# Optimization experiments

Measured on AMD Instinct MI355X. Metric: run time of the kernel, lower is better.

## Reference

```python
import jax, jax.numpy as jnp
import numpy as np

DN = ('NCHW', 'OIHW', 'NCHW')

def conv2d(x, w, b):
    y = jax.lax.conv_general_dilated(x, w, (1, 1), 'SAME', dimension_numbers=DN)
    return y + b[None, :, None, None]

def deform_conv2d(x, offset, w, b):
    # torchvision DeformConv2d v1: kernel 3x3, stride 1, pad 1, dilation 1, no mask.
    # offset: [B, 18, H, W] ordered (dy0, dx0, dy1, dx1, ...) over row-major kernel taps.
    B, C, H, W = x.shape
    K2 = 9
    ki = (jnp.arange(K2) // 3).astype(x.dtype)  # kernel row index i
    kj = (jnp.arange(K2) % 3).astype(x.dtype)   # kernel col index j
    dy = offset[:, 0::2]  # [B, 9, H, W]
    dx = offset[:, 1::2]
    hh = jnp.arange(H, dtype=x.dtype)
    ww = jnp.arange(W, dtype=x.dtype)
    # sampling positions: p = out_pos - pad + k + offset
    py = hh[None, None, :, None] + ki[None, :, None, None] - 1.0 + dy  # [B,9,H,W]
    px = ww[None, None, None, :] + kj[None, :, None, None] - 1.0 + dx

    xf = x.reshape(B, C, H * W)
    y0 = jnp.floor(py); x0 = jnp.floor(px)
    y1 = y0 + 1.0;      x1 = x0 + 1.0
    wy1 = py - y0; wy0 = 1.0 - wy1
    wx1 = px - x0; wx0 = 1.0 - wx1

    def corner(yc, xc, cw):
        valid = (yc >= 0) & (yc <= H - 1) & (xc >= 0) & (xc <= W - 1)
        yi = jnp.clip(yc, 0, H - 1).astype(jnp.int32)
        xi = jnp.clip(xc, 0, W - 1).astype(jnp.int32)
        idx = yi * W + xi                       # [B,9,H,W]
        v = jax.vmap(lambda img, i: img[:, i])(xf, idx)  # [B,C,9,H,W]
        return v * (cw * valid.astype(x.dtype))[:, None]

    sampled = (corner(y0, x0, wy0 * wx0) + corner(y0, x1, wy0 * wx1)
               + corner(y1, x0, wy1 * wx0) + corner(y1, x1, wy1 * wx1))  # [B,C,9,H,W]
    out = jnp.einsum('bckhw,ock->bohw', sampled, w.reshape(w.shape[0], C, K2))
    return out + b[None, :, None, None]

def setup_inputs() -> dict:
    key = jax.random.key(0)
    ks = jax.random.split(key, 20)
    B, C, H, W = 8, 64, 128, 128
    O = 64
    s = 0.05
    inp = {
        'x': jax.random.normal(ks[0], (B, C, H, W), jnp.float32),
        'bsize': jax.random.uniform(ks[1], (B, 2), jnp.float32),
        # glob: Linear(2,64) -> ReLU -> Linear(64,32)
        'gw1': s * jax.random.normal(ks[2], (64, 2), jnp.float32),
        'gb1': jnp.zeros((64,), jnp.float32),
        'gw2': s * jax.random.normal(ks[3], (32, 64), jnp.float32),
        'gb2': jnp.zeros((32,), jnp.float32),
        # local: Conv2d(C,32,3) -> ReLU -> Conv2d(32,32,3)
        'lw1': s * jax.random.normal(ks[4], (32, C, 3, 3), jnp.float32),
        'lb1': jnp.zeros((32,), jnp.float32),
        'lw2': s * jax.random.normal(ks[5], (32, 32, 3, 3), jnp.float32),
        'lb2': jnp.zeros((32,), jnp.float32),
        # fuse: Conv2d(64,32,3) -> ReLU -> Conv2d(32,18,3)
        'fw1': s * jax.random.normal(ks[6], (32, 64, 3, 3), jnp.float32),
        'fb1': jnp.zeros((32,), jnp.float32),
        'fw2': s * jax.random.normal(ks[7], (18, 32, 3, 3), jnp.float32),
        'fb2': jnp.zeros((18,), jnp.float32),
        # deformable conv weight (copied from the source nn.Conv2d) + its own bias
        'dw': s * jax.random.normal(ks[8], (O, C, 3, 3), jnp.float32),
        'db': jnp.zeros((O,), jnp.float32),
    }
    return inp

def reference(x, bsize, gw1, gb1, gw2, gb2, lw1, lb1, lw2, lb2,
              fw1, fb1, fw2, fb2, dw, db):
    B, C, H, W = x.shape
    # global branch: MLP on box-size -> broadcast over spatial dims
    g = jax.nn.relu(bsize @ gw1.T + gb1) @ gw2.T + gb2          # [B,32]
    g_offset = jnp.broadcast_to(g[:, :, None, None], (B, 32, H, W))
    # local branch
    l_offset = conv2d(jax.nn.relu(conv2d(x, lw1, lb1)), lw2, lb2)  # [B,32,H,W]
    # fuse -> 18 offset channels
    fused = jnp.concatenate((g_offset, l_offset), axis=1)          # [B,64,H,W]
    offset = conv2d(jax.nn.relu(conv2d(fused, fw1, fb1)), fw2, fb2)  # [B,18,H,W]
    fea = deform_conv2d(x, offset, dw, db)
    return jax.nn.relu(fea)
```

## Files before the change

### kernel.cpp

```cpp
#include <hip/hip_runtime.h>

#define BB 8
#define CC 64
#define HH 128
#define WW 128
#define HWSZ (HH*WW)

typedef _Float16 h16;
typedef __attribute__((ext_vector_type(8))) _Float16 h16x8;
typedef __attribute__((ext_vector_type(4))) _Float16 h16x4;
typedef __attribute__((ext_vector_type(2))) _Float16 h16x2;
typedef __attribute__((ext_vector_type(4))) float f32x4;

typedef const __attribute__((address_space(1))) unsigned int* gptr_t;
typedef __attribute__((address_space(3))) unsigned int* lptr_t;

__device__ __forceinline__ void conv_pack(int j, int NCG, const float* w,
                                          int maxo, h16* dst) {
  int e = j & 7, l4 = (j >> 3) & 3, l15 = (j >> 5) & 15, f = (j >> 9) & 1;
  int cg = (j >> 10) & (NCG - 1), kt = (j >> 10) / NCG;
  int o = f * 16 + l15, c = cg * 32 + l4 * 8 + e;
  int CINw = NCG * 32;
  dst[j] = (o < maxo) ? (h16)w[(o * CINw + c) * 9 + kt] : (h16)0.f;
}

__global__ __launch_bounds__(256) void prep_kernel(
    const float* __restrict__ bsize, const float* __restrict__ gw1,
    const float* __restrict__ gb1, const float* __restrict__ gw2,
    const float* __restrict__ gb2, float* __restrict__ g,
    const float* __restrict__ lw1, const float* __restrict__ lw2,
    const float* __restrict__ fw1, const float* __restrict__ fw2,
    const float* __restrict__ dw, h16* __restrict__ cwq,
    h16* __restrict__ dwq, const float* __restrict__ x,
    h16* __restrict__ xt) {
  __shared__ float hbuf[BB][64];
  const int blk = blockIdx.x;
  const int tid = threadIdx.x;
  if (blk == 0) {
#pragma unroll
    for (int i2 = 0; i2 < 2; ++i2) {
      int idx = i2 * 256 + tid;
      int b = idx >> 6, i = idx & 63;
      float v = fmaf(bsize[b * 2 + 0], gw1[i * 2 + 0],
                     fmaf(bsize[b * 2 + 1], gw1[i * 2 + 1], gb1[i]));
      hbuf[b][i] = fmaxf(v, 0.f);
    }
    __syncthreads();
    int b = tid >> 5, j = tid & 31;
    float acc = gb2[j];
#pragma unroll
    for (int i = 0; i < 64; ++i) acc = fmaf(hbuf[b][i], gw2[j * 64 + i], acc);
    g[b * 32 + j] = acc;
  } else if (blk <= 360) {
    int i = (blk - 1) * 256 + tid;
    if (i < 18432) {
      conv_pack(i, 2, lw1, 32, cwq);
    } else if (i < 27648) {
      conv_pack(i - 18432, 1, lw2, 32, cwq + 18432);
    } else if (i < 46080) {
      conv_pack(i - 27648, 2, fw1, 32, cwq + 27648);
    } else if (i < 55296) {
      conv_pack(i - 46080, 1, fw2, 18, cwq + 46080);
    } else if (i < 55296 + 36864) {
      int j = i - 55296;
      int e = j & 7, l4 = (j >> 3) & 3, l15 = (j >> 5) & 15;
      int og = (j >> 9) & 3, cg = (j >> 11) & 1, kt = j >> 12;
      int o = og * 16 + l15, c = cg * 32 + l4 * 8 + e;
      dwq[j] = (h16)dw[(o * 64 + c) * 9 + kt];
    }
  } else {
    int j = blk - 361;
    int b = (1 + j) & 7;
    int slot = j >> 3;
    int t = b * 16384 + slot * 256 + tid;
    int p = t & 16383;
    const float* xb = x + (size_t)b * 64 * HWSZ + p;
    h16* ob = xt + (size_t)t * 64;
#pragma unroll
    for (int c0 = 0; c0 < 64; c0 += 8) {
      h16x8 v;
#pragma unroll
      for (int i = 0; i < 8; ++i) v[i] = (h16)xb[(size_t)(c0 + i) * HWSZ];
      *(h16x8*)(ob + c0) = v;
    }
  }
}

template <int NCG, bool GFUSE, bool RELU, int OMODE>
__global__ __launch_bounds__(512) void conv_mfma_kernel(
    const h16* __restrict__ in, const h16* __restrict__ cwq,
    const float* __restrict__ bias, const float* __restrict__ g,
    h16* __restrict__ outv) {
  constexpr int CINS = GFUSE ? 32 : NCG * 32;
  constexpr int NS = CINS / 8;
  constexpr int LOG2NS = (NS == 8) ? 3 : 2;
  constexpr int NCHUNK = 4 * 128 * NS;
  __shared__ __align__(16) h16 sh[4 * 128 * CINS];
  const int wgid = (blockIdx.x & 7) * 64 + (blockIdx.x >> 3);
  const int b = wgid >> 6;
  const int h0 = (wgid & 63) * 2;
  const int lane = threadIdx.x & 63, wave = threadIdx.x >> 6;
  const int wr = wave >> 2, wv = wave & 3;
  const int h = h0 + wr;
  const int l15 = lane & 15, l4 = lane >> 4;
  const h16* inb = in + (size_t)b * HWSZ * CINS;

#pragma unroll
  for (int it = 0; it < NCHUNK / 512; ++it) {
    int q = it * 512 + threadIdx.x;
    int sp = q & (NS - 1), pr = q >> LOG2NS;
    int r = pr >> 7, px = pr & 127;
    int gy = min(max(h0 - 1 + r, 0), HH - 1);
    int s = sp ^ (px & (NS - 1));
    const h16* src = inb + ((size_t)gy * WW + px) * CINS + s * 8;
    __builtin_amdgcn_global_load_lds(
        (gptr_t)src, (lptr_t)(sh + (size_t)(it * 512 + wave * 64) * 8), 16, 0, 0);
  }

  const h16x8 zfr = {0, 0, 0, 0, 0, 0, 0, 0};
  h16x8 gfr = zfr;
  if (GFUSE) {
#pragma unroll
    for (int i = 0; i < 8; ++i) gfr[i] = (h16)g[b * 32 + l4 * 8 + i];
  }
  __syncthreads();

  f32x4 acc[2][2];
#pragma unroll
  for (int f = 0; f < 2; ++f)
#pragma unroll
    for (int j = 0; j < 2; ++j) acc[f][j] = (f32x4){0.f, 0.f, 0.f, 0.f};

#pragma unroll
  for (int kt = 0; kt < 9; ++kt) {
    const int ki = kt / 3 - 1, kj = kt % 3 - 1;
    const int y = h + ki;
    const bool yok = (unsigned)y < HH;
    const int r = ki + 1 + wr;
    int xs[2];
    bool ok[2];
#pragma unroll
    for (int j = 0; j < 2; ++j) {
      int xx = wv * 32 + j * 16 + l15 + kj;
      ok[j] = yok && ((unsigned)xx < WW);
      xs[j] = min(max(xx, 0), WW - 1);
    }
#pragma unroll
    for (int cg = 0; cg < NCG; ++cg) {
      const h16* aq = cwq + (size_t)((kt * NCG + cg) * 2) * 512 + l15 * 32 + l4 * 8;
      h16x8 afr0 = *(const h16x8*)(aq);
      h16x8 afr1 = *(const h16x8*)(aq + 512);
#pragma unroll
      for (int j = 0; j < 2; ++j) {
        h16x8 bv;
        if (GFUSE && cg == 0) {
          bv = ok[j] ? gfr : zfr;
        } else {
          const int s = (!GFUSE && NCG == 2) ? cg * 4 + l4 : l4;
          h16x8 ld = *(const h16x8*)(sh + (r * 128 + xs[j]) * CINS +
                                     ((s ^ (xs[j] & (NS - 1))) * 8));
          bv = ok[j] ? ld : zfr;
        }
        acc[0][j] = __builtin_amdgcn_mfma_f32_16x16x32_f16(afr0, bv, acc[0][j], 0, 0, 0);
        acc[1][j] = __builtin_amdgcn_mfma_f32_16x16x32_f16(afr1, bv, acc[1][j], 0, 0, 0);
      }
    }
  }
  if (OMODE == 0) {
    h16* ob = outv + (size_t)b * HWSZ * 32;
#pragma unroll
    for (int f = 0; f < 2; ++f)
#pragma unroll
      for (int j = 0; j < 2; ++j) {
        int p = h * WW + wv * 32 + j * 16 + l15;
        int o0 = f * 16 + l4 * 4;
        h16x4 st;
#pragma unroll
        for (int r2 = 0; r2 < 4; ++r2) {
          float v = acc[f][j][r2] + bias[o0 + r2];
          if (RELU) v = fmaxf(v, 0.f);
          st[r2] = (h16)v;
        }
        *(h16x4*)(ob + (size_t)p * 32 + o0) = st;
      }
  } else {
    h16* ob = outv + (size_t)b * HWSZ * 24;
#pragma unroll
    for (int j = 0; j < 2; ++j) {
      int p = h * WW + wv * 32 + j * 16 + l15;
      {
        int o0 = l4 * 4;
        h16x4 st;
#pragma unroll
        for (int r2 = 0; r2 < 4; ++r2) st[r2] = (h16)(acc[0][j][r2] + bias[o0 + r2]);
        *(h16x4*)(ob + (size_t)p * 24 + o0) = st;
      }
      if (l4 == 0) {
        h16x2 st2;
        st2[0] = (h16)(acc[1][j][0] + bias[16]);
        st2[1] = (h16)(acc[1][j][1] + bias[17]);
        *(h16x2*)(ob + (size_t)p * 24 + 16) = st2;
      }
    }
  }
}

__global__ __launch_bounds__(256) void deform_mfma_kernel(
    const h16* __restrict__ xt, const h16* __restrict__ offc,
    const h16* __restrict__ dwq, const float* __restrict__ db,
    float* __restrict__ out) {
  __shared__ __align__(16) h16 sh[5 * 72 * 64];
  const int wgid = (blockIdx.x & 7) * 256 + (blockIdx.x >> 3);
  const int b = wgid >> 8;
  const int rh = wgid & 255;
  const int h = rh >> 1;
  const int halfx = (rh & 1) * 64;
  const int x_lo = halfx - 4;
  const int lane = threadIdx.x & 63, wave = threadIdx.x >> 6;
  const int l15 = lane & 15, l4 = lane >> 4;
  const int wx = halfx + wave * 16;
  const int p0 = h * WW + wx;
  const int myw = wx + l15;
  const int mypix = p0 + l15;
  const h16* xb = xt + (size_t)b * HWSZ * 64;

#pragma unroll
  for (int it = 0; it < 12; ++it) {
    int q = it * 256 + threadIdx.x;
    if (q < 2880) {
      int sp = q & 7, pr = q >> 3;
      int r = pr / 72, i = pr - r * 72;
      int gy = min(max(h - 2 + r, 0), HH - 1);
      int gx = min(max(x_lo + i, 0), WW - 1);
      int s = sp ^ (i & 7);
      const h16* src = xb + ((size_t)gy * WW + gx) * 64 + s * 8;
      __builtin_amdgcn_global_load_lds(
          (gptr_t)src, (lptr_t)(sh + (size_t)(it * 256 + wave * 64) * 8), 16, 0, 0);
    }
  }

  const h16* offp = offc + ((size_t)b * HWSZ + mypix) * 24;
  h16x8 offv0 = *(const h16x8*)(offp);
  h16x8 offv1 = *(const h16x8*)(offp + 8);
  h16x8 offv2 = *(const h16x8*)(offp + 16);
  __syncthreads();

#define OFFE(e) ((e) < 8 ? (float)offv0[(e) & 7] : (e) < 16 ? (float)offv1[(e) & 7] : (float)offv2[(e) & 7])

  f32x4 acc[4];
#pragma unroll
  for (int og = 0; og < 4; ++og) acc[og] = (f32x4){0.f, 0.f, 0.f, 0.f};

  h16x8 pc[2][2][4];
  h16x8 pw[2][8];
  h16   pg[2][4];

#define PREF(kt, par) do {                                                  \
    float py = (float)(h + (kt) / 3 - 1) + OFFE(2 * (kt));                  \
    float px = (float)(myw + (kt) % 3 - 1) + OFFE(2 * (kt) + 1);            \
    float y0f = floorf(py), x0f = floorf(px);                               \
    float wy1 = py - y0f, wy0 = 1.f - wy1;                                  \
    float wx1 = px - x0f, wx0 = 1.f - wx1;                                  \
    int y0 = (int)y0f, x0i = (int)x0f;                                      \
    int y1 = y0 + 1, x1i = x0i + 1;                                         \
    bool y0ok = (unsigned)y0 < HH, y1ok = (unsigned)y1 < HH;                \
    bool x0ok = (unsigned)x0i < WW, x1ok = (unsigned)x1i < WW;              \
    pg[par][0] = (h16)((y0ok && x0ok) ? wy0 * wx0 : 0.f);                   \
    pg[par][1] = (h16)((y0ok && x1ok) ? wy0 * wx1 : 0.f);                   \
    pg[par][2] = (h16)((y1ok && x0ok) ? wy1 * wx0 : 0.f);                   \
    pg[par][3] = (h16)((y1ok && x1ok) ? wy1 * wx1 : 0.f);                   \
    int y0c = min(max(y0, 0), HH - 1), y1c = min(max(y1, 0), HH - 1);       \
    int x0c = min(max(x0i, 0), WW - 1), x1c = min(max(x1i, 0), WW - 1);     \
    int ty0u = y0c - (h - 2), ty1u = y1c - (h - 2);                         \
    int tx0u = x0c - x_lo, tx1u = x1c - x_lo;                               \
    bool fast = ((unsigned)ty0u <= 4u) & ((unsigned)ty1u <= 4u) &           \
                ((unsigned)tx0u <= 71u) & ((unsigned)tx1u <= 71u);          \
    int ty0 = min(max(ty0u, 0), 4), ty1 = min(max(ty1u, 0), 4);             \
    int tx0 = min(max(tx0u, 0), 71), tx1 = min(max(tx1u, 0), 71);           \
    int pr00 = (ty0 * 72 + tx0) * 64, pr01 = (ty0 * 72 + tx1) * 64;         \
    int pr10 = (ty1 * 72 + tx0) * 64, pr11 = (ty1 * 72 + tx1) * 64;         \
    int sx0 = (tx0 & 7) * 8, sx1 = (tx1 & 7) * 8;                           \
    _Pragma("unroll")                                                       \
    for (int cg = 0; cg < 2; ++cg) {                                        \
      int sb = (cg * 4 + l4) * 8;                                           \
      pc[par][cg][0] = *(const h16x8*)(sh + pr00 + (sb ^ sx0));             \
      pc[par][cg][1] = *(const h16x8*)(sh + pr01 + (sb ^ sx1));             \
      pc[par][cg][2] = *(const h16x8*)(sh + pr10 + (sb ^ sx0));             \
      pc[par][cg][3] = *(const h16x8*)(sh + pr11 + (sb ^ sx1));             \
    }                                                                       \
    if (!fast) {                                                            \
      int i00 = y0c * WW + x0c, i01 = y0c * WW + x1c;                       \
      int i10 = y1c * WW + x0c, i11 = y1c * WW + x1c;                       \
      _Pragma("unroll")                                                     \
      for (int cg = 0; cg < 2; ++cg) {                                      \
        const h16* cb = xb + cg * 32 + l4 * 8;                              \
        pc[par][cg][0] = *(const h16x8*)(cb + (size_t)i00 * 64);            \
        pc[par][cg][1] = *(const h16x8*)(cb + (size_t)i01 * 64);            \
        pc[par][cg][2] = *(const h16x8*)(cb + (size_t)i10 * 64);            \
        pc[par][cg][3] = *(const h16x8*)(cb + (size_t)i11 * 64);            \
      }                                                                     \
    }                                                                       \
    const h16* wq0 = dwq + ((size_t)((kt) * 2 + 0) * 64 + l15) * 32 + l4 * 8; \
    const h16* wq1 = dwq + ((size_t)((kt) * 2 + 1) * 64 + l15) * 32 + l4 * 8; \
    pw[par][0] = *(const h16x8*)(wq0 + 0 * 512);                            \
    pw[par][1] = *(const h16x8*)(wq0 + 1 * 512);                            \
    pw[par][2] = *(const h16x8*)(wq0 + 2 * 512);                            \
    pw[par][3] = *(const h16x8*)(wq0 + 3 * 512);                            \
    pw[par][4] = *(const h16x8*)(wq1 + 0 * 512);                            \
    pw[par][5] = *(const h16x8*)(wq1 + 1 * 512);                            \
    pw[par][6] = *(const h16x8*)(wq1 + 2 * 512);                            \
    pw[par][7] = *(const h16x8*)(wq1 + 3 * 512);                            \
  } while (0)

#define CONS(par) do {                                                      \
    h16 w00 = pg[par][0], w01 = pg[par][1], w10 = pg[par][2], w11 = pg[par][3]; \
    h16x8 s0 = pc[par][0][0] * w00 + pc[par][0][1] * w01                    \
             + pc[par][0][2] * w10 + pc[par][0][3] * w11;                   \
    h16x8 s1 = pc[par][1][0] * w00 + pc[par][1][1] * w01                    \
             + pc[par][1][2] * w10 + pc[par][1][3] * w11;                   \
    acc[0] = __builtin_amdgcn_mfma_f32_16x16x32_f16(s0, pw[par][0], acc[0], 0, 0, 0); \
    acc[1] = __builtin_amdgcn_mfma_f32_16x16x32_f16(s0, pw[par][1], acc[1], 0, 0, 0); \
    acc[2] = __builtin_amdgcn_mfma_f32_16x16x32_f16(s0, pw[par][2], acc[2], 0, 0, 0); \
    acc[3] = __builtin_amdgcn_mfma_f32_16x16x32_f16(s0, pw[par][3], acc[3], 0, 0, 0); \
    acc[0] = __builtin_amdgcn_mfma_f32_16x16x32_f16(s1, pw[par][4], acc[0], 0, 0, 0); \
    acc[1] = __builtin_amdgcn_mfma_f32_16x16x32_f16(s1, pw[par][5], acc[1], 0, 0, 0); \
    acc[2] = __builtin_amdgcn_mfma_f32_16x16x32_f16(s1, pw[par][6], acc[2], 0, 0, 0); \
    acc[3] = __builtin_amdgcn_mfma_f32_16x16x32_f16(s1, pw[par][7], acc[3], 0, 0, 0); \
  } while (0)

  PREF(0, 0);
  PREF(1, 1);
  CONS(0);
  PREF(2, 0);
  CONS(1);
  PREF(3, 1);
  CONS(0);
  PREF(4, 0);
  CONS(1);
  PREF(5, 1);
  CONS(0);
  PREF(6, 0);
  CONS(1);
  PREF(7, 1);
  CONS(0);
  PREF(8, 0);
  CONS(1);
  CONS(0);
#undef PREF
#undef CONS
#undef OFFE

  float* outb = out + (size_t)b * CC * HWSZ;
#pragma unroll
  for (int og = 0; og < 4; ++og) {
    int o = og * 16 + l15;
    float bv = db[o];
    f32x4 st;
#pragma unroll
    for (int r = 0; r < 4; ++r) st[r] = fmaxf(acc[og][r] + bv, 0.f);
    *(f32x4*)(outb + (size_t)o * HWSZ + p0 + l4 * 4) = st;
  }
}

extern "C" void kernel_launch(void* const* d_in, const int* in_sizes, int n_in,
                              void* d_out, int out_size, void* d_ws, size_t ws_size,
                              hipStream_t stream) {
  const float* x     = (const float*)d_in[0];
  const float* bsize = (const float*)d_in[1];
  const float* gw1   = (const float*)d_in[2];
  const float* gb1   = (const float*)d_in[3];
  const float* gw2   = (const float*)d_in[4];
  const float* gb2   = (const float*)d_in[5];
  const float* lw1   = (const float*)d_in[6];
  const float* lb1   = (const float*)d_in[7];
  const float* lw2   = (const float*)d_in[8];
  const float* lb2   = (const float*)d_in[9];
  const float* fw1   = (const float*)d_in[10];
  const float* fb1   = (const float*)d_in[11];
  const float* fw2   = (const float*)d_in[12];
  const float* fb2   = (const float*)d_in[13];
  const float* dw    = (const float*)d_in[14];
  const float* db    = (const float*)d_in[15];
  float* out = (float*)d_out;

  float* gbuf = (float*)d_ws;
  h16* xt   = (h16*)((char*)d_ws + 2048);
  h16* offc = (h16*)((char*)d_ws + 2048 + (size_t)BB * HWSZ * 64 * 2);
  h16* dwq  = (h16*)((char*)offc + (size_t)BB * HWSZ * 24 * 2);

  h16* loff = (h16*)d_out;
  h16* cwq  = (h16*)d_out + 4194304;
  h16* t12  = (h16*)d_out + 8388608;
  const h16* lw1q = cwq;
  const h16* lw2q = cwq + 18432;
  const h16* fw1q = cwq + 27648;
  const h16* fw2q = cwq + 46080;

  prep_kernel<<<873, 256, 0, stream>>>(bsize, gw1, gb1, gw2, gb2, gbuf,
                                       lw1, lw2, fw1, fw2, dw, cwq, dwq, x, xt);
  conv_mfma_kernel<2, false, true, 0><<<512, 512, 0, stream>>>(
      xt, lw1q, lb1, nullptr, t12);
  conv_mfma_kernel<1, false, false, 0><<<512, 512, 0, stream>>>(
      t12, lw2q, lb2, nullptr, loff);
  conv_mfma_kernel<2, true, true, 0><<<512, 512, 0, stream>>>(
      loff, fw1q, fb1, gbuf, t12);
  conv_mfma_kernel<1, false, false, 1><<<512, 512, 0, stream>>>(
      t12, fw2q, fb2, nullptr, offc);
  deform_mfma_kernel<<<2048, 256, 0, stream>>>(xt, offc, dwq, db, out);
}
```

Baseline: 102.1 us.

## Fuse final offset conv into deformable conv kernel when workspace allows

The last 3x3 conv producing the 18 offset channels is computed inside the deformable conv kernel. Each block stages a 3-row halo of the 32-channel intermediate into LDS, runs MFMAs against packed fw2 weights, and passes the offsets through shared memory. This removes one kernel launch and the write and re-read of the offset tensor. In exchange it adds extra LDS, barriers and some halo recompute to the deform kernel, and it only takes effect if the workspace is large enough.

```diff
diff --git a/kernel.cpp b/kernel.cpp
--- a/kernel.cpp
+++ b/kernel.cpp
@@ -31,8 +31,8 @@
     const float* __restrict__ lw1, const float* __restrict__ lw2,
     const float* __restrict__ fw1, const float* __restrict__ fw2,
     const float* __restrict__ dw, h16* __restrict__ cwq,
-    h16* __restrict__ dwq, const float* __restrict__ x,
-    h16* __restrict__ xt) {
+    h16* __restrict__ dwq, h16* __restrict__ fw2w,
+    const float* __restrict__ x, h16* __restrict__ xt) {
   __shared__ float hbuf[BB][64];
   const int blk = blockIdx.x;
   const int tid = threadIdx.x;
@@ -61,6 +61,7 @@
       conv_pack(i - 27648, 2, fw1, 32, cwq + 27648);
     } else if (i < 55296) {
       conv_pack(i - 46080, 1, fw2, 18, cwq + 46080);
+      conv_pack(i - 46080, 1, fw2, 18, fw2w);
     } else if (i < 55296 + 36864) {
       int j = i - 55296;
       int e = j & 7, l4 = (j >> 3) & 3, l15 = (j >> 5) & 15;
@@ -205,11 +206,14 @@
   }
 }
 
+template <bool FUSED>
 __global__ __launch_bounds__(256) void deform_mfma_kernel(
-    const h16* __restrict__ xt, const h16* __restrict__ offc,
+    const h16* __restrict__ xt, const h16* __restrict__ aux,
     const h16* __restrict__ dwq, const float* __restrict__ db,
+    const h16* __restrict__ fw2q, const float* __restrict__ fb2,
     float* __restrict__ out) {
   __shared__ __align__(16) h16 sh[5 * 72 * 64];
+  __shared__ __align__(16) h16 sh2[FUSED ? 3 * 72 * 32 : 8];
   const int wgid = (blockIdx.x & 7) * 256 + (blockIdx.x >> 3);
   const int b = wgid >> 8;
   const int rh = wgid & 255;
@@ -223,6 +227,7 @@
   const int myw = wx + l15;
   const int mypix = p0 + l15;
   const h16* xb = xt + (size_t)b * HWSZ * 64;
+  const h16x8 zfr8 = {0, 0, 0, 0, 0, 0, 0, 0};
 
 #pragma unroll
   for (int it = 0; it < 12; ++it) {
@@ -239,13 +244,66 @@
     }
   }
 
-  const h16* offp = offc + ((size_t)b * HWSZ + mypix) * 24;
-  h16x8 offv0 = *(const h16x8*)(offp);
-  h16x8 offv1 = *(const h16x8*)(offp + 8);
-  h16x8 offv2 = *(const h16x8*)(offp + 16);
-  __syncthreads();
-
-#define OFFE(e) ((e) < 8 ? (float)offv0[(e) & 7] : (e) < 16 ? (float)offv1[(e) & 7] : (float)offv2[(e) & 7])
+  float offr[18];
+  if constexpr (FUSED) {
+    const h16* t2b = aux + (size_t)b * HWSZ * 32;
+#pragma unroll
+    for (int it = 0; it < 4; ++it) {
+      int q = it * 256 + threadIdx.x;
+      if (q < 864) {
+        int sp = q & 3, pr = q >> 2;
+        int r = pr / 72, i = pr - r * 72;
+        int gy = min(max(h - 1 + r, 0), HH - 1);
+        int gx = min(max(halfx - 1 + i, 0), WW - 1);
+        int s = sp ^ (i & 3);
+        const h16* src = t2b + ((size_t)gy * WW + gx) * 32 + s * 8;
+        __builtin_amdgcn_global_load_lds(
+            (gptr_t)src, (lptr_t)(sh2 + (size_t)(it * 256 + wave * 64) * 8), 16, 0, 0);
+      }
+    }
+    __syncthreads();
+    f32x4 oa0 = (f32x4){0.f, 0.f, 0.f, 0.f};
+    f32x4 oa1 = (f32x4){0.f, 0.f, 0.f, 0.f};
+#pragma unroll
+    for (int kt = 0; kt < 9; ++kt) {
+      const int ki = kt / 3 - 1, kj = kt % 3 - 1;
+      int y = h + ki;
+      int xx = wx + l15 + kj;
+      bool ok = ((unsigned)y < HH) && ((unsigned)xx < WW);
+      int txc = min(max(xx, 0), WW - 1) - (halfx - 1);
+      h16x8 av = ok ? *(const h16x8*)(sh2 + ((ki + 1) * 72 + txc) * 32 +
+                                      ((l4 ^ (txc & 3)) * 8))
+                    : zfr8;
+      h16x8 w0 = *(const h16x8*)(fw2q + kt * 1024 + l15 * 32 + l4 * 8);
+      h16x8 w1 = *(const h16x8*)(fw2q + kt * 1024 + 512 + l15 * 32 + l4 * 8);
+      oa0 = __builtin_amdgcn_mfma_f32_16x16x32_f16(w0, av, oa0, 0, 0, 0);
+      oa1 = __builtin_amdgcn_mfma_f32_16x16x32_f16(w1, av, oa1, 0, 0, 0);
+    }
+    __syncthreads();
+    float* shf2 = (float*)sh2;
+#pragma unroll
+    for (int r = 0; r < 4; ++r) {
+      int o = l4 * 4 + r;
+      shf2[(wave * 16 + l15) * 20 + o] = oa0[r] + fb2[o];
+    }
+    if (l4 == 0) {
+      shf2[(wave * 16 + l15) * 20 + 16] = oa1[0] + fb2[16];
+      shf2[(wave * 16 + l15) * 20 + 17] = oa1[1] + fb2[17];
+    }
+    __syncthreads();
+#pragma unroll
+    for (int e = 0; e < 18; ++e) offr[e] = shf2[(wave * 16 + l15) * 20 + e];
+  } else {
+    const h16* offp = aux + ((size_t)b * HWSZ + mypix) * 24;
+    h16x8 offv0 = *(const h16x8*)(offp);
+    h16x8 offv1 = *(const h16x8*)(offp + 8);
+    h16x8 offv2 = *(const h16x8*)(offp + 16);
+    __syncthreads();
+#pragma unroll
+    for (int e = 0; e < 18; ++e)
+      offr[e] = (e < 8) ? (float)offv0[e & 7]
+              : (e < 16) ? (float)offv1[e & 7] : (float)offv2[e & 7];
+  }
 
   f32x4 acc[4];
 #pragma unroll
@@ -256,8 +314,8 @@
   h16   pg[2][4];
 
 #define PREF(kt, par) do {                                                  \
-    float py = (float)(h + (kt) / 3 - 1) + OFFE(2 * (kt));                  \
-    float px = (float)(myw + (kt) % 3 - 1) + OFFE(2 * (kt) + 1);            \
+    float py = (float)(h + (kt) / 3 - 1) + offr[2 * (kt)];                  \
+    float px = (float)(myw + (kt) % 3 - 1) + offr[2 * (kt) + 1];            \
     float y0f = floorf(py), x0f = floorf(px);                               \
     float wy1 = py - y0f, wy0 = 1.f - wy1;                                  \
     float wx1 = px - x0f, wx0 = 1.f - wx1;                                  \
@@ -348,7 +406,6 @@
   CONS(0);
 #undef PREF
 #undef CONS
-#undef OFFE
 
   float* outb = out + (size_t)b * CC * HWSZ;
 #pragma unroll
@@ -383,10 +440,27 @@
   const float* db    = (const float*)d_in[15];
   float* out = (float*)d_out;
 
+  const size_t XT  = (size_t)BB * HWSZ * 64 * 2;
+  const size_t T2  = (size_t)BB * HWSZ * 32 * 2;
+  const size_t OFC = (size_t)BB * HWSZ * 24 * 2;
+  const size_t DWQ = 36864 * 2;
+  const size_t FW2 = 9216 * 2;
+  const bool fused = ws_size >= 2048 + XT + T2 + DWQ + FW2;
+
   float* gbuf = (float*)d_ws;
-  h16* xt   = (h16*)((char*)d_ws + 2048);
-  h16* offc = (h16*)((char*)d_ws + 2048 + (size_t)BB * HWSZ * 64 * 2);
-  h16* dwq  = (h16*)((char*)offc + (size_t)BB * HWSZ * 24 * 2);
+  h16* xt = (h16*)((char*)d_ws + 2048);
+  h16 *t2ws, *offc, *dwq, *fw2w;
+  if (fused) {
+    t2ws = (h16*)((char*)xt + XT);
+    dwq  = (h16*)((char*)t2ws + T2);
+    fw2w = (h16*)((char*)dwq + DWQ);
+    offc = nullptr;
+  } else {
+    offc = (h16*)((char*)xt + XT);
+    dwq  = (h16*)((char*)offc + OFC);
+    fw2w = offc;
+    t2ws = nullptr;
+  }
 
   h16* loff = (h16*)d_out;
   h16* cwq  = (h16*)d_out + 4194304;
@@ -397,14 +471,22 @@
   const h16* fw2q = cwq + 46080;
 
   prep_kernel<<<873, 256, 0, stream>>>(bsize, gw1, gb1, gw2, gb2, gbuf,
-                                       lw1, lw2, fw1, fw2, dw, cwq, dwq, x, xt);
+                                       lw1, lw2, fw1, fw2, dw, cwq, dwq, fw2w, x, xt);
   conv_mfma_kernel<2, false, true, 0><<<512, 512, 0, stream>>>(
       xt, lw1q, lb1, nullptr, t12);
   conv_mfma_kernel<1, false, false, 0><<<512, 512, 0, stream>>>(
       t12, lw2q, lb2, nullptr, loff);
-  conv_mfma_kernel<2, true, true, 0><<<512, 512, 0, stream>>>(
-      loff, fw1q, fb1, gbuf, t12);
-  conv_mfma_kernel<1, false, false, 1><<<512, 512, 0, stream>>>(
-      t12, fw2q, fb2, nullptr, offc);
-  deform_mfma_kernel<<<2048, 256, 0, stream>>>(xt, offc, dwq, db, out);
+  if (fused) {
+    conv_mfma_kernel<2, true, true, 0><<<512, 512, 0, stream>>>(
+        loff, fw1q, fb1, gbuf, t2ws);
+    deform_mfma_kernel<true><<<2048, 256, 0, stream>>>(
+        xt, t2ws, dwq, db, fw2w, fb2, out);
+  } else {
+    conv_mfma_kernel<2, true, true, 0><<<512, 512, 0, stream>>>(
+        loff, fw1q, fb1, gbuf, t12);
+    conv_mfma_kernel<1, false, false, 1><<<512, 512, 0, stream>>>(
+        t12, fw2q, fb2, nullptr, offc);
+    deform_mfma_kernel<false><<<2048, 256, 0, stream>>>(
+        xt, offc, dwq, db, nullptr, nullptr, out);
+  }
 }
```

New measurement: 103.9 us. No clear change (+1.8%).
